# Kernel optimization log

Measured on AMD Instinct MI355X. Metric: run time of the kernel, lower is better.

The kernel has to match this reference:

```python
import jax, jax.numpy as jnp
import numpy as np

D_MODEL, D_STATE, D_CONV, EXPAND = 2048, 16, 4, 2
D_INNER = EXPAND * D_MODEL            # 4096
DT_RANK = -(-D_MODEL // 16)           # 128
B_SZ, L = 2, 1024


def setup_inputs() -> dict:
    key = jax.random.key(0)
    ks = jax.random.split(key, 10)
    s = 0.02
    return {
        "hidden_states": jax.random.normal(ks[0], (B_SZ, L, D_MODEL), jnp.float32),
        "in_proj_w": jax.random.normal(ks[1], (2 * D_INNER, D_MODEL), jnp.float32) * s,
        "conv_w": jax.random.normal(ks[2], (D_INNER, D_CONV), jnp.float32) * 0.1,
        "conv_b": jax.random.normal(ks[3], (D_INNER,), jnp.float32) * 0.1,
        "x_proj_w": jax.random.normal(ks[4], (DT_RANK + 2 * D_STATE, D_INNER), jnp.float32) * s,
        "dt_proj_w": jax.random.normal(ks[5], (D_INNER, DT_RANK), jnp.float32) * s,
        "dt_proj_b": jax.random.normal(ks[6], (D_INNER,), jnp.float32) * 0.1 - 4.0,
        "A": -jax.random.uniform(ks[7], (D_INNER, D_STATE), jnp.float32, 1.0, 16.0),
        "D": jnp.ones((D_INNER,), jnp.float32),
        "out_proj_w": jax.random.normal(ks[8], (D_MODEL, D_INNER), jnp.float32) * s,
    }


def _mamba_forward(hidden_states, in_proj_w, conv_w, conv_b, x_proj_w,
                   dt_proj_w, dt_proj_b, A, D, out_proj_w):
    # in_proj: [B,L,d_model] -> [B,L,2*d_inner]; chunk into x and gate
    proj = jnp.einsum('bld,ed->ble', hidden_states, in_proj_w)
    x, gate = jnp.split(proj, 2, axis=-1)            # each [B,L,d_inner]

    # depthwise causal conv1d over time + SiLU
    xc = x.transpose(0, 2, 1)                        # [B,d_inner,L]
    xc = jax.lax.conv_general_dilated(
        xc, conv_w[:, None, :],                      # kernel [d_inner,1,d_conv]
        window_strides=(1,), padding=[(D_CONV - 1, 0)],
        feature_group_count=D_INNER,
        dimension_numbers=('NCH', 'OIH', 'NCH'))
    xc = jax.nn.silu(xc + conv_b[None, :, None])
    xt = xc.transpose(0, 2, 1)                       # [B,L,d_inner]

    # x_proj -> (dt_rank, d_state, d_state)
    ssm = jnp.einsum('bld,ed->ble', xt, x_proj_w)
    ts, Bm, Cm = jnp.split(ssm, [DT_RANK, DT_RANK + D_STATE], axis=-1)
    dt = jnp.einsum('blr,dr->bld', ts, dt_proj_w)    # dt_proj (skip_bias_add)
    dt = jax.nn.softplus(dt + dt_proj_b)             # delta_softplus with bias

    # selective scan over time
    def step(state, inp):
        dt_t, x_t, B_t, C_t = inp                    # [B,di],[B,di],[B,ds],[B,ds]
        dA = jnp.exp(dt_t[..., None] * A)            # [B,d_inner,d_state]
        dBx = dt_t[..., None] * B_t[:, None, :] * x_t[..., None]
        state = state * dA + dBx
        y = jnp.einsum('bds,bs->bd', state, C_t)
        return state, y

    xs = (dt.transpose(1, 0, 2), xt.transpose(1, 0, 2),
          Bm.transpose(1, 0, 2), Cm.transpose(1, 0, 2))
    state0 = jnp.zeros((hidden_states.shape[0], D_INNER, D_STATE), jnp.float32)
    _, ys = jax.lax.scan(step, state0, xs)           # [L,B,d_inner]
    y = ys.transpose(1, 0, 2) + xt * D               # D skip connection
    y = y * jax.nn.silu(gate)                        # gating (z in selective scan)

    return jnp.einsum('bld,ed->ble', y, out_proj_w)  # out_proj -> [B,L,d_model]


def reference(hidden_states, in_proj_w, conv_w, conv_b, x_proj_w,
              dt_proj_w, dt_proj_b, A, D, out_proj_w):
    return _mamba_forward(hidden_states, in_proj_w, conv_w, conv_b, x_proj_w,
                          dt_proj_w, dt_proj_b, A, D, out_proj_w)
```

## Files before the change

### kernel.cpp

```cpp
#include <hip/hip_runtime.h>
#include <hip/hip_bf16.h>
#include <math.h>

#define B_SZ    2
#define LSEQ    1024
#define D_MODEL 2048
#define D_INNER 4096
#define D_STATE 16
#define DT_RANK 128
#define M_TOK   (B_SZ * LSEQ)
#define NCHUNK  16
#define LCHUNK  (LSEQ / NCHUNK)

typedef __attribute__((ext_vector_type(8))) short bf16x8;
typedef __attribute__((ext_vector_type(4))) float f32x4;

__device__ __forceinline__ float softplusf_(float x) {
    return fmaxf(x, 0.f) + log1pf(expf(-fabsf(x)));
}
__device__ __forceinline__ unsigned f2bf(float f) {
    union { float f; unsigned u; } v; v.f = f;
    const unsigned u = v.u;
    return (u + 0x7fffu + ((u >> 16) & 1u)) >> 16;
}
__device__ __forceinline__ float bf2f(unsigned u) {
    union { unsigned u; float f; } v; v.u = u << 16; return v.f;
}
__device__ __forceinline__ void gload16(const void* g, void* lds) {
    __builtin_amdgcn_global_load_lds(
        (const __attribute__((address_space(1))) void*)g,
        (__attribute__((address_space(3))) void*)lds, 16, 0, 0);
}

__global__ __launch_bounds__(512, 2)
void gemm256_1ph(const ushort* __restrict__ A, int lda,
                 const ushort* __restrict__ B, int ldb,
                 void* __restrict__ Cv, int ldc,
                 void* __restrict__ Cv2,
                 int K, int epi, size_t zstride)
{
    __shared__ ushort Lds[2][2][2][128 * 64];
    const int t    = threadIdx.x;
    const int bm   = blockIdx.y << 8, bn = blockIdx.x << 8;
    const int wave = t >> 6, lane = t & 63;
    const int wm   = wave >> 2;
    const int wn   = wave & 3;
    const int lr   = lane & 15, lh = lane >> 4;
    const int kper  = K / gridDim.z;
    const int kbase = blockIdx.z * kper;
    const int nkt   = kper >> 6;

    const ushort* gsA[2]; const ushort* gsB[2];
    int dof[2];
#pragma unroll
    for (int it = 0; it < 2; ++it) {
        const int flat = t + (it << 9);
        const int row  = flat >> 3, j = flat & 7;
        const int jj   = j ^ (row & 7);
        gsA[it] = A + (size_t)(bm + row) * lda + kbase + jj * 8;
        gsB[it] = B + (size_t)(bn + row) * ldb + kbase + jj * 8;
        dof[it] = flat << 3;
    }

#define STG_A(half, kt, db) do {                                            \
    _Pragma("unroll")                                                       \
    for (int it = 0; it < 2; ++it)                                          \
        gload16(gsA[it] + (size_t)((half) * 128) * lda + (kt) * 64,         \
                &Lds[db][0][half][dof[it]]);                                \
} while (0)
#define STG_B(half, kt, db) do {                                            \
    _Pragma("unroll")                                                       \
    for (int it = 0; it < 2; ++it)                                          \
        gload16(gsB[it] + (size_t)((half) * 128) * ldb + (kt) * 64,         \
                &Lds[db][1][half][dof[it]]);                                \
} while (0)
#define RD_A(db, half) do {                                                 \
    _Pragma("unroll")                                                       \
    for (int mi = 0; mi < 4; ++mi)                                          \
    _Pragma("unroll")                                                       \
    for (int kk = 0; kk < 2; ++kk) {                                        \
        const int row_ = wm * 64 + mi * 16 + lr;                            \
        const int ch_  = ((kk << 2) + lh) ^ (row_ & 7);                     \
        af[mi * 2 + kk] = *(const bf16x8*)((const char*)Lds[db][0][half]    \
                             + row_ * 128 + (ch_ << 4));                    \
    }                                                                       \
} while (0)
#define RD_B(db, half, dst) do {                                            \
    _Pragma("unroll")                                                       \
    for (int nj = 0; nj < 2; ++nj)                                          \
    _Pragma("unroll")                                                       \
    for (int kk = 0; kk < 2; ++kk) {                                        \
        const int row_ = wn * 32 + nj * 16 + lr;                            \
        const int ch_  = ((kk << 2) + lh) ^ (row_ & 7);                     \
        dst[nj * 2 + kk] = *(const bf16x8*)((const char*)Lds[db][1][half]   \
                             + row_ * 128 + (ch_ << 4));                    \
    }                                                                       \
} while (0)
#define MFMA_PAIR(qa, qb, bfa, bfb) do {                                    \
    _Pragma("unroll")                                                       \
    for (int kk = 0; kk < 2; ++kk) {                                        \
        _Pragma("unroll")                                                   \
        for (int mi = 0; mi < 4; ++mi)                                      \
        _Pragma("unroll")                                                   \
        for (int nj = 0; nj < 2; ++nj)                                      \
            acc[qa][mi][nj] = __builtin_amdgcn_mfma_f32_16x16x32_bf16(      \
                af[mi * 2 + kk], bfa[nj * 2 + kk], acc[qa][mi][nj], 0, 0, 0);\
        _Pragma("unroll")                                                   \
        for (int mi = 0; mi < 4; ++mi)                                      \
        _Pragma("unroll")                                                   \
        for (int nj = 0; nj < 2; ++nj)                                      \
            acc[qb][mi][nj] = __builtin_amdgcn_mfma_f32_16x16x32_bf16(      \
                af[mi * 2 + kk], bfb[nj * 2 + kk], acc[qb][mi][nj], 0, 0, 0);\
    }                                                                       \
} while (0)

    f32x4 acc[4][4][2];
#pragma unroll
    for (int q = 0; q < 4; ++q)
#pragma unroll
        for (int i = 0; i < 4; ++i)
#pragma unroll
            for (int j = 0; j < 2; ++j) {
                acc[q][i][j][0] = 0.f; acc[q][i][j][1] = 0.f;
                acc[q][i][j][2] = 0.f; acc[q][i][j][3] = 0.f;
            }

    bf16x8 af[8], bf0[4], bf1[4];

    STG_A(0, 0, 0); STG_B(0, 0, 0); STG_B(1, 0, 0); STG_A(1, 0, 0);
    asm volatile("s_waitcnt vmcnt(0)" ::: "memory");
    __builtin_amdgcn_s_barrier();

    for (int kt = 0; kt < nkt; ++kt) {
        const int db = kt & 1;
        RD_A(db, 0); RD_B(db, 0, bf0); RD_B(db, 1, bf1);
        if (kt + 1 < nkt) {
            STG_A(0, kt + 1, db ^ 1); STG_B(0, kt + 1, db ^ 1);
            STG_B(1, kt + 1, db ^ 1); STG_A(1, kt + 1, db ^ 1);
        }
        MFMA_PAIR(0, 1, bf0, bf1);
        RD_A(db, 1);
        MFMA_PAIR(2, 3, bf1, bf0);
        asm volatile("s_waitcnt vmcnt(0)" ::: "memory");
        __builtin_amdgcn_s_barrier();
    }
#undef STG_A
#undef STG_B
#undef RD_A
#undef RD_B
#undef MFMA_PAIR

    float*  C  = (float*)Cv + (size_t)blockIdx.z * zstride;
    ushort* Cb = (ushort*)Cv;
    ushort* C2 = (ushort*)Cv2;
#pragma unroll
    for (int q = 0; q < 4; ++q) {
        const int mh = q >> 1;
        const int nh = (q == 1 || q == 2) ? 1 : 0;
#pragma unroll
        for (int mi = 0; mi < 4; ++mi) {
#pragma unroll
            for (int nj = 0; nj < 2; ++nj) {
                const int col  = bn + nh * 128 + wn * 32 + nj * 16 + lr;
                const int row0 = bm + mh * 128 + wm * 64 + mi * 16 + (lh << 2);
#pragma unroll
                for (int r = 0; r < 4; ++r) {
                    const float v = acc[q][mi][nj][r];
                    if (epi == 0) {
                        C[(size_t)(row0 + r) * ldc + col] = v;
                    } else {
                        if (col < D_INNER)
                            Cb[(size_t)(row0 + r) * ldc + col] = (ushort)f2bf(v);
                        else
                            C2[(size_t)(row0 + r) * ldc + (col - D_INNER)] = (ushort)f2bf(v);
                    }
                }
            }
        }
    }
}

__global__ __launch_bounds__(512, 4)
void gemm_bf16_bt(const ushort* __restrict__ A, int lda,
                  const ushort* __restrict__ B, int ldb,
                  void* __restrict__ Cv, int ldc,
                  const float* __restrict__ bias,
                  int M, int N, int K, int epi, size_t zstride)
{
    __shared__ ushort As[2][128 * 64];
    __shared__ ushort Bs[2][128 * 64];
    const int t    = threadIdx.x;
    const int bm   = blockIdx.y << 7, bn = blockIdx.x << 7;
    const int wave = t >> 6, lane = t & 63;
    const int wr   = (wave >> 2) << 6;
    const int wc   = (wave & 3) << 5;
    const int lr   = lane & 15, lh = lane >> 4;
    const int kper  = K / gridDim.z;
    const int kbase = blockIdx.z * kper;
    const int nkt   = kper >> 6;

    const ushort* ga[2]; const ushort* gb[2];
    int ldof[2];
#pragma unroll
    for (int it = 0; it < 2; ++it) {
        const int seg = wave + (it << 3);
        const int row = (seg << 3) + (lane >> 3);
        const int jj  = (lane & 7) ^ ((lane >> 3) & 7);
        ga[it] = A + (size_t)(bm + row) * lda + kbase + jj * 8;
        int gn = bn + row; gn = gn < N ? gn : N - 1;
        gb[it] = B + (size_t)gn * ldb + kbase + jj * 8;
        ldof[it] = seg << 9;
    }

#define STAGE(bsel) do {                                                \
    _Pragma("unroll")                                                   \
    for (int it = 0; it < 2; ++it) {                                    \
        gload16(ga[it], &As[bsel][ldof[it]]);                           \
        gload16(gb[it], &Bs[bsel][ldof[it]]);                           \
        ga[it] += 64; gb[it] += 64;                                     \
    }                                                                   \
} while (0)

    f32x4 acc[4][2];
#pragma unroll
    for (int i = 0; i < 4; ++i)
#pragma unroll
        for (int j = 0; j < 2; ++j) {
            acc[i][j][0] = 0.f; acc[i][j][1] = 0.f;
            acc[i][j][2] = 0.f; acc[i][j][3] = 0.f;
        }

    STAGE(0);
    for (int kt = 0; kt < nkt; ++kt) {
        const int cur = kt & 1;
        if (kt + 1 < nkt) {
            STAGE(cur ^ 1);
            asm volatile("s_waitcnt vmcnt(4)" ::: "memory");
        } else {
            asm volatile("s_waitcnt vmcnt(0)" ::: "memory");
        }
        __builtin_amdgcn_s_barrier();

        const char* Ab = (const char*)As[cur];
        const char* Bb = (const char*)Bs[cur];
#pragma unroll
        for (int kk = 0; kk < 2; ++kk) {
            bf16x8 af[4], bf[2];
#pragma unroll
            for (int mi = 0; mi < 4; ++mi) {
                const int row = wr + (mi << 4) + lr;
                const int ch  = ((kk << 2) + lh) ^ (row & 7);
                af[mi] = *(const bf16x8*)(Ab + row * 128 + (ch << 4));
            }
#pragma unroll
            for (int nj = 0; nj < 2; ++nj) {
                const int row = wc + (nj << 4) + lr;
                const int ch  = ((kk << 2) + lh) ^ (row & 7);
                bf[nj] = *(const bf16x8*)(Bb + row * 128 + (ch << 4));
            }
#pragma unroll
            for (int mi = 0; mi < 4; ++mi)
#pragma unroll
                for (int nj = 0; nj < 2; ++nj)
                    acc[mi][nj] = __builtin_amdgcn_mfma_f32_16x16x32_bf16(
                        af[mi], bf[nj], acc[mi][nj], 0, 0, 0);
        }
        __builtin_amdgcn_s_barrier();
    }
#undef STAGE

    float*  C  = (float*)Cv + (size_t)blockIdx.z * zstride;
    ushort* Cb = (ushort*)Cv;
#pragma unroll
    for (int mi = 0; mi < 4; ++mi) {
#pragma unroll
        for (int nj = 0; nj < 2; ++nj) {
            const int col  = bn + wc + (nj << 4) + lr;
            const int row0 = bm + wr + (mi << 4) + (lh << 2);
            if (col < N) {
#pragma unroll
                for (int r = 0; r < 4; ++r) {
                    const float v = acc[mi][nj][r];
                    if (epi == 0)
                        C[(size_t)(row0 + r) * ldc + col] = v;
                    else
                        Cb[(size_t)(row0 + r) * ldc + col] =
                            (ushort)f2bf(softplusf_(v + bias[col]));
                }
            }
        }
    }
}

#define CVT_N_HS   524288
#define CVT_N_INW  2097152
#define CVT1_E0    (CVT_N_HS)
#define CVT1_E1    (CVT1_E0 + CVT_N_INW)

__global__ __launch_bounds__(256)
void cvt_step1(const float* __restrict__ hs,  ushort* __restrict__ hsb,
               const float* __restrict__ inw, ushort* __restrict__ inwb)
{
    for (int i = blockIdx.x * 256 + threadIdx.x; i < CVT1_E1; i += gridDim.x * 256) {
        const float* in; ushort* out; int j;
        if (i < CVT1_E0) { in = hs;  out = hsb;  j = i; }
        else             { in = inw; out = inwb; j = i - CVT1_E0; }
        const float4 v0 = ((const float4*)in)[j * 2];
        const float4 v1 = ((const float4*)in)[j * 2 + 1];
        int4 p;
        p.x = (int)(f2bf(v0.x) | (f2bf(v0.y) << 16));
        p.y = (int)(f2bf(v0.z) | (f2bf(v0.w) << 16));
        p.z = (int)(f2bf(v1.x) | (f2bf(v1.y) << 16));
        p.w = (int)(f2bf(v1.z) | (f2bf(v1.w) << 16));
        ((int4*)out)[j] = p;
    }
}

#define CVT_N_OW   1048576
#define CVT_N_XW   81920
#define CVT_N_DTW  65536
#define CVT4_E0    (CVT_N_OW)
#define CVT4_E1    (CVT4_E0 + CVT_N_XW)
#define CVT4_E2    (CVT4_E1 + CVT_N_DTW)

__global__ __launch_bounds__(256)
void cvt_step4(const float* __restrict__ ow,  ushort* __restrict__ owb,
               const float* __restrict__ xw,  ushort* __restrict__ xwb,
               const float* __restrict__ dtw, ushort* __restrict__ dtwb)
{
    for (int i = blockIdx.x * 256 + threadIdx.x; i < CVT4_E2; i += gridDim.x * 256) {
        const float* in; ushort* out; int j;
        if (i < CVT4_E0)      { in = ow;  out = owb;  j = i; }
        else if (i < CVT4_E1) { in = xw;  out = xwb;  j = i - CVT4_E0; }
        else                  { in = dtw; out = dtwb; j = i - CVT4_E1; }
        const float4 v0 = ((const float4*)in)[j * 2];
        const float4 v1 = ((const float4*)in)[j * 2 + 1];
        int4 p;
        p.x = (int)(f2bf(v0.x) | (f2bf(v0.y) << 16));
        p.y = (int)(f2bf(v0.z) | (f2bf(v0.w) << 16));
        p.z = (int)(f2bf(v1.x) | (f2bf(v1.y) << 16));
        p.w = (int)(f2bf(v1.z) | (f2bf(v1.w) << 16));
        ((int4*)out)[j] = p;
    }
}

__global__ __launch_bounds__(256)
void reduce_out4(const float* __restrict__ part, float* __restrict__ out, int n4)
{
    const int stride = M_TOK * D_MODEL / 4;
    for (int i = blockIdx.x * 256 + threadIdx.x; i < n4; i += gridDim.x * 256) {
        const float4 a = ((const float4*)part)[i];
        const float4 b = ((const float4*)part)[i + stride];
        const float4 c = ((const float4*)part)[i + 2 * stride];
        const float4 d = ((const float4*)part)[i + 3 * stride];
        ((float4*)out)[i] = make_float4(a.x + b.x + c.x + d.x,
                                        a.y + b.y + c.y + d.y,
                                        a.z + b.z + c.z + d.z,
                                        a.w + b.w + c.w + d.w);
    }
}

__global__ __launch_bounds__(256)
void conv_silu_k(const ushort* __restrict__ xraw,
                 const float* __restrict__ cw,
                 const float* __restrict__ cb,
                 ushort* __restrict__ xb)
{
    const int d  = (blockIdx.x << 8) + threadIdx.x;
    const int m0 = blockIdx.y << 6;
    const int l0 = m0 & (LSEQ - 1);
    const float4 w = *(const float4*)&cw[d << 2];
    const float bias = cb[d];
    float x3 = 0.f, x2 = 0.f, x1 = 0.f;
    if (l0 > 0) {
        x3 = bf2f(xraw[(size_t)(m0 - 3) * D_INNER + d]);
        x2 = bf2f(xraw[(size_t)(m0 - 2) * D_INNER + d]);
        x1 = bf2f(xraw[(size_t)(m0 - 1) * D_INNER + d]);
    }
#pragma unroll 4
    for (int i = 0; i < 64; ++i) {
        const size_t m = (size_t)m0 + i;
        const float x0 = bf2f(xraw[m * D_INNER + d]);
        float acc = bias;
        acc = fmaf(w.x, x3, acc);
        acc = fmaf(w.y, x2, acc);
        acc = fmaf(w.z, x1, acc);
        acc = fmaf(w.w, x0, acc);
        const float sg = 1.f / (1.f + expf(-acc));
        xb[m * D_INNER + d] = (ushort)f2bf(acc * sg);
        x3 = x2; x2 = x1; x1 = x0;
    }
}

__global__ __launch_bounds__(256)
void reduce_ssm(const float* __restrict__ part,
                float* __restrict__ ssmf, ushort* __restrict__ ssmb)
{
    const int i = blockIdx.x * 256 + threadIdx.x;
    float v = 0.f;
#pragma unroll
    for (int z = 0; z < 8; ++z) v += part[(size_t)z * (M_TOK * 160) + i];
    ssmf[i] = v;
    ssmb[i] = (ushort)f2bf(v);
}

__global__ __launch_bounds__(256)
void scan_pass1(const ushort* __restrict__ dtp,
                const ushort* __restrict__ xb,
                const float* __restrict__ ssm,
                const float* __restrict__ Ap,
                float* __restrict__ Pc, float* __restrict__ Qc)
{
    const int d = (blockIdx.x << 8) + threadIdx.x;
    const int c = blockIdx.y, b = blockIdx.z;
    float a[16];
    *(float4*)&a[0]  = *(const float4*)&Ap[d * 16];
    *(float4*)&a[4]  = *(const float4*)&Ap[d * 16 + 4];
    *(float4*)&a[8]  = *(const float4*)&Ap[d * 16 + 8];
    *(float4*)&a[12] = *(const float4*)&Ap[d * 16 + 12];
    float q[16];
#pragma unroll
    for (int s = 0; s < 16; ++s) q[s] = 0.f;
    float dtsum = 0.f;
    const size_t m0 = (size_t)b * LSEQ + (size_t)c * LCHUNK;
#pragma unroll 2
    for (int l = 0; l < LCHUNK; ++l) {
        const size_t m = m0 + l;
        const float dt = bf2f(dtp[m * D_INNER + d]);
        const float xv = bf2f(xb[m * D_INNER + d]);
        const float4 B0 = *(const float4*)&ssm[m * 160 + 128];
        const float4 B1 = *(const float4*)&ssm[m * 160 + 132];
        const float4 B2 = *(const float4*)&ssm[m * 160 + 136];
        const float4 B3 = *(const float4*)&ssm[m * 160 + 140];
        const float Bv[16] = {B0.x,B0.y,B0.z,B0.w, B1.x,B1.y,B1.z,B1.w,
                              B2.x,B2.y,B2.z,B2.w, B3.x,B3.y,B3.z,B3.w};
        const float t1 = dt * xv;
#pragma unroll
        for (int s = 0; s < 16; ++s) {
            const float dA = __expf(dt * a[s]);
            q[s] = fmaf(q[s], dA, t1 * Bv[s]);
        }
        dtsum += dt;
    }
    const size_t o = (((size_t)b * D_INNER + d) * NCHUNK + c) * D_STATE;
    float P[16];
#pragma unroll
    for (int s = 0; s < 16; ++s) P[s] = __expf(a[s] * dtsum);
#pragma unroll
    for (int s4 = 0; s4 < 4; ++s4) {
        *(float4*)&Pc[o + s4 * 4] = make_float4(P[s4*4], P[s4*4+1], P[s4*4+2], P[s4*4+3]);
        *(float4*)&Qc[o + s4 * 4] = make_float4(q[s4*4], q[s4*4+1], q[s4*4+2], q[s4*4+3]);
    }
}

__global__ __launch_bounds__(256)
void scan_pass2(const float* __restrict__ Pc, float* __restrict__ Qc)
{
    const int i = blockIdx.x * 256 + threadIdx.x;
    const size_t base = (size_t)(i >> 4) * (NCHUNK * D_STATE) + (i & 15);
    float st = 0.f;
#pragma unroll
    for (int c = 0; c < NCHUNK; ++c) {
        const float P = Pc[base + c * D_STATE];
        const float q = Qc[base + c * D_STATE];
        Qc[base + c * D_STATE] = st;
        st = fmaf(st, P, q);
    }
}

__global__ __launch_bounds__(256)
void scan_pass3(const ushort* __restrict__ dtp,
                ushort* __restrict__ xb,
                const ushort* __restrict__ gb,
                const float* __restrict__ ssm,
                const float* __restrict__ Ap,
                const float* __restrict__ Qc,
                const float* __restrict__ Dp)
{
    const int d = (blockIdx.x << 8) + threadIdx.x;
    const int c = blockIdx.y, b = blockIdx.z;
    float a[16], st[16];
    *(float4*)&a[0]  = *(const float4*)&Ap[d * 16];
    *(float4*)&a[4]  = *(const float4*)&Ap[d * 16 + 4];
    *(float4*)&a[8]  = *(const float4*)&Ap[d * 16 + 8];
    *(float4*)&a[12] = *(const float4*)&Ap[d * 16 + 12];
    const size_t qo = (((size_t)b * D_INNER + d) * NCHUNK + c) * D_STATE;
    *(float4*)&st[0]  = *(const float4*)&Qc[qo];
    *(float4*)&st[4]  = *(const float4*)&Qc[qo + 4];
    *(float4*)&st[8]  = *(const float4*)&Qc[qo + 8];
    *(float4*)&st[12] = *(const float4*)&Qc[qo + 12];
    const float Dd = Dp[d];
    const size_t m0 = (size_t)b * LSEQ + (size_t)c * LCHUNK;
#pragma unroll 2
    for (int l = 0; l < LCHUNK; ++l) {
        const size_t m = m0 + l;
        const float dt = bf2f(dtp[m * D_INNER + d]);
        const float xv = bf2f(xb[m * D_INNER + d]);
        const float gv = bf2f(gb[m * D_INNER + d]);
        const float4 B0 = *(const float4*)&ssm[m * 160 + 128];
        const float4 B1 = *(const float4*)&ssm[m * 160 + 132];
        const float4 B2 = *(const float4*)&ssm[m * 160 + 136];
        const float4 B3 = *(const float4*)&ssm[m * 160 + 140];
        const float4 C0 = *(const float4*)&ssm[m * 160 + 144];
        const float4 C1 = *(const float4*)&ssm[m * 160 + 148];
        const float4 C2 = *(const float4*)&ssm[m * 160 + 152];
        const float4 C3 = *(const float4*)&ssm[m * 160 + 156];
        const float Bv[16] = {B0.x,B0.y,B0.z,B0.w, B1.x,B1.y,B1.z,B1.w,
                              B2.x,B2.y,B2.z,B2.w, B3.x,B3.y,B3.z,B3.w};
        const float Cv[16] = {C0.x,C0.y,C0.z,C0.w, C1.x,C1.y,C1.z,C1.w,
                              C2.x,C2.y,C2.z,C2.w, C3.x,C3.y,C3.z,C3.w};
        const float t1 = dt * xv;
        float y = 0.f;
#pragma unroll
        for (int s = 0; s < 16; ++s) {
            const float dA = __expf(dt * a[s]);
            st[s] = fmaf(st[s], dA, t1 * Bv[s]);
            y = fmaf(st[s], Cv[s], y);
        }
        const float yg  = fmaf(Dd, xv, y);
        const float sig = 1.f / (1.f + expf(-gv));
        xb[m * D_INNER + d] = (ushort)f2bf(yg * (gv * sig));
    }
}

extern "C" void kernel_launch(void* const* d_in, const int* in_sizes, int n_in,
                              void* d_out, int out_size, void* d_ws, size_t ws_size,
                              hipStream_t stream)
{
    (void)in_sizes; (void)n_in; (void)out_size; (void)ws_size;
    const float* hs  = (const float*)d_in[0];
    const float* inw = (const float*)d_in[1];
    const float* cw  = (const float*)d_in[2];
    const float* cb  = (const float*)d_in[3];
    const float* xw  = (const float*)d_in[4];
    const float* dtw = (const float*)d_in[5];
    const float* dtb = (const float*)d_in[6];
    const float* Ap  = (const float*)d_in[7];
    const float* Dp  = (const float*)d_in[8];
    const float* ow  = (const float*)d_in[9];
    float* out = (float*)d_out;

    float*  ws    = (float*)d_ws;
    float*  P     = ws;
    ushort* hsb   = (ushort*)(ws + 0);
    ushort* inwb  = (ushort*)(ws + 2097152);
    ushort* dtb16 = (ushort*)(ws + 0);
    ushort* xwb   = (ushort*)(ws + 4194304);
    ushort* dtwb  = (ushort*)(ws + 4521984);
    float*  ssmf  = ws + 4784128;
    ushort* ssmb  = (ushort*)(ws + 5111808);
    float*  part  = ws + 5275648;
    float*  Pc    = ws + 5275648;
    float*  Qc    = ws + 7372800;
    ushort* pg    = (ushort*)(ws + 10485760);
    ushort* xtb   = (ushort*)(ws + 16777216);
    ushort* xraw  = (ushort*)(ws + 20971520);
    ushort* owb   = (ushort*)(ws + 20971520);

    const dim3 blk(256);
    const dim3 blk512(512);

    cvt_step1<<<dim3(2048), blk, 0, stream>>>(hs, hsb, inw, inwb);

    gemm256_1ph<<<dim3(32, 8, 1), blk512, 0, stream>>>(
        hsb, D_MODEL, inwb, D_MODEL, xraw, D_INNER, pg, D_MODEL, 5, 0);

    conv_silu_k<<<dim3(16, 32), blk, 0, stream>>>(xraw, cw, cb, xtb);

    cvt_step4<<<dim3(2048), blk, 0, stream>>>(ow, owb, xw, xwb, dtw, dtwb);

    gemm_bf16_bt<<<dim3(2, 16, 8), blk512, 0, stream>>>(
        xtb, D_INNER, xwb, D_INNER, part, 160, nullptr,
        M_TOK, 160, D_INNER, 0, (size_t)M_TOK * 160);
    reduce_ssm<<<dim3(1280), blk, 0, stream>>>(part, ssmf, ssmb);

    gemm_bf16_bt<<<dim3(32, 16, 1), blk512, 0, stream>>>(
        ssmb, 160, dtwb, DT_RANK, dtb16, D_INNER, dtb,
        M_TOK, D_INNER, DT_RANK, 1, 0);

    scan_pass1<<<dim3(16, NCHUNK, B_SZ), blk, 0, stream>>>(dtb16, xtb, ssmf, Ap, Pc, Qc);
    scan_pass2<<<dim3((B_SZ * D_INNER * D_STATE) / 256), blk, 0, stream>>>(Pc, Qc);
    scan_pass3<<<dim3(16, NCHUNK, B_SZ), blk, 0, stream>>>(dtb16, xtb, pg, ssmf, Ap, Qc, Dp);

    gemm256_1ph<<<dim3(8, 8, 4), blk512, 0, stream>>>(
        xtb, D_INNER, owb, D_INNER, P, D_MODEL, nullptr,
        D_INNER, 0, (size_t)M_TOK * D_MODEL);
    reduce_out4<<<dim3(1024), blk, 0, stream>>>(P, out, (M_TOK * D_MODEL) / 4);
}
```

Before: 300.7 us.

## Fuse three chunked selective-scan passes into one kernel with LDS carry propagation

Replaces the three-kernel chunked scan (per-chunk local scan, cross-chunk prefix, final scan with output) with a single kernel. Each block owns 16 channels across all 16 chunks and keeps chunk decay and partial states in shared memory. A block-local sequential pass over chunks computes the carry-in states between two barriers. This removes two kernel launches and the global write and re-read of the Pc/Qc chunk-state buffers. In exchange, each wavefront now reads only 16 contiguous channels per token row across four different chunks, so global loads of dt, x and gate are less coalesced.

```diff
diff --git a/kernel.cpp b/kernel.cpp
--- a/kernel.cpp
+++ b/kernel.cpp
@@ -405,24 +405,32 @@
 }
 
 __global__ __launch_bounds__(256)
-void scan_pass1(const ushort* __restrict__ dtp,
-                const ushort* __restrict__ xb,
+void scan_fused(const ushort* __restrict__ dtp,
+                ushort* __restrict__ xb,
+                const ushort* __restrict__ gb,
                 const float* __restrict__ ssm,
                 const float* __restrict__ Ap,
-                float* __restrict__ Pc, float* __restrict__ Qc)
-{
-    const int d = (blockIdx.x << 8) + threadIdx.x;
-    const int c = blockIdx.y, b = blockIdx.z;
+                const float* __restrict__ Dp)
+{
+    __shared__ float Pl[16 * 17 * 16];
+    __shared__ float Ql[16 * 17 * 16];
+    const int t  = threadIdx.x;
+    const int dl = t & 15, c = t >> 4;
+    const int d  = (blockIdx.x << 4) + dl;
+    const int b  = blockIdx.y;
+    const int base = (dl * 17 + c) * 16;
+
     float a[16];
     *(float4*)&a[0]  = *(const float4*)&Ap[d * 16];
     *(float4*)&a[4]  = *(const float4*)&Ap[d * 16 + 4];
     *(float4*)&a[8]  = *(const float4*)&Ap[d * 16 + 8];
     *(float4*)&a[12] = *(const float4*)&Ap[d * 16 + 12];
+    const size_t m0 = (size_t)b * LSEQ + (size_t)c * LCHUNK;
+
     float q[16];
 #pragma unroll
     for (int s = 0; s < 16; ++s) q[s] = 0.f;
     float dtsum = 0.f;
-    const size_t m0 = (size_t)b * LSEQ + (size_t)c * LCHUNK;
 #pragma unroll 2
     for (int l = 0; l < LCHUNK; ++l) {
         const size_t m = m0 + l;
@@ -442,55 +450,38 @@
         }
         dtsum += dt;
     }
-    const size_t o = (((size_t)b * D_INNER + d) * NCHUNK + c) * D_STATE;
-    float P[16];
-#pragma unroll
-    for (int s = 0; s < 16; ++s) P[s] = __expf(a[s] * dtsum);
 #pragma unroll
     for (int s4 = 0; s4 < 4; ++s4) {
-        *(float4*)&Pc[o + s4 * 4] = make_float4(P[s4*4], P[s4*4+1], P[s4*4+2], P[s4*4+3]);
-        *(float4*)&Qc[o + s4 * 4] = make_float4(q[s4*4], q[s4*4+1], q[s4*4+2], q[s4*4+3]);
-    }
-}
-
-__global__ __launch_bounds__(256)
-void scan_pass2(const float* __restrict__ Pc, float* __restrict__ Qc)
-{
-    const int i = blockIdx.x * 256 + threadIdx.x;
-    const size_t base = (size_t)(i >> 4) * (NCHUNK * D_STATE) + (i & 15);
-    float st = 0.f;
-#pragma unroll
-    for (int c = 0; c < NCHUNK; ++c) {
-        const float P = Pc[base + c * D_STATE];
-        const float q = Qc[base + c * D_STATE];
-        Qc[base + c * D_STATE] = st;
-        st = fmaf(st, P, q);
-    }
-}
-
-__global__ __launch_bounds__(256)
-void scan_pass3(const ushort* __restrict__ dtp,
-                ushort* __restrict__ xb,
-                const ushort* __restrict__ gb,
-                const float* __restrict__ ssm,
-                const float* __restrict__ Ap,
-                const float* __restrict__ Qc,
-                const float* __restrict__ Dp)
-{
-    const int d = (blockIdx.x << 8) + threadIdx.x;
-    const int c = blockIdx.y, b = blockIdx.z;
-    float a[16], st[16];
-    *(float4*)&a[0]  = *(const float4*)&Ap[d * 16];
-    *(float4*)&a[4]  = *(const float4*)&Ap[d * 16 + 4];
-    *(float4*)&a[8]  = *(const float4*)&Ap[d * 16 + 8];
-    *(float4*)&a[12] = *(const float4*)&Ap[d * 16 + 12];
-    const size_t qo = (((size_t)b * D_INNER + d) * NCHUNK + c) * D_STATE;
-    *(float4*)&st[0]  = *(const float4*)&Qc[qo];
-    *(float4*)&st[4]  = *(const float4*)&Qc[qo + 4];
-    *(float4*)&st[8]  = *(const float4*)&Qc[qo + 8];
-    *(float4*)&st[12] = *(const float4*)&Qc[qo + 12];
+        float4 Pv;
+        Pv.x = __expf(a[s4 * 4 + 0] * dtsum);
+        Pv.y = __expf(a[s4 * 4 + 1] * dtsum);
+        Pv.z = __expf(a[s4 * 4 + 2] * dtsum);
+        Pv.w = __expf(a[s4 * 4 + 3] * dtsum);
+        *(float4*)&Pl[base + s4 * 4] = Pv;
+        *(float4*)&Ql[base + s4 * 4] = make_float4(q[s4*4], q[s4*4+1],
+                                                   q[s4*4+2], q[s4*4+3]);
+    }
+    __syncthreads();
+
+    {
+        const int dl2 = t >> 4, s2 = t & 15;
+        float st2 = 0.f;
+#pragma unroll
+        for (int c2 = 0; c2 < NCHUNK; ++c2) {
+            const int idx = (dl2 * 17 + c2) * 16 + s2;
+            const float Pv = Pl[idx];
+            const float qv = Ql[idx];
+            Ql[idx] = st2;
+            st2 = fmaf(st2, Pv, qv);
+        }
+    }
+    __syncthreads();
+
+    float st[16];
+#pragma unroll
+    for (int s4 = 0; s4 < 4; ++s4)
+        *(float4*)&st[s4 * 4] = *(const float4*)&Ql[base + s4 * 4];
     const float Dd = Dp[d];
-    const size_t m0 = (size_t)b * LSEQ + (size_t)c * LCHUNK;
 #pragma unroll 2
     for (int l = 0; l < LCHUNK; ++l) {
         const size_t m = m0 + l;
@@ -550,8 +541,6 @@
     float*  ssmf  = ws + 4784128;
     ushort* ssmb  = (ushort*)(ws + 5111808);
     float*  part  = ws + 5275648;
-    float*  Pc    = ws + 5275648;
-    float*  Qc    = ws + 7372800;
     ushort* pg    = (ushort*)(ws + 10485760);
     ushort* xtb   = (ushort*)(ws + 16777216);
     ushort* xraw  = (ushort*)(ws + 20971520);
@@ -578,9 +567,8 @@
         ssmb, 160, dtwb, DT_RANK, dtb16, D_INNER, dtb,
         M_TOK, D_INNER, DT_RANK, 1, 0);
 
-    scan_pass1<<<dim3(16, NCHUNK, B_SZ), blk, 0, stream>>>(dtb16, xtb, ssmf, Ap, Pc, Qc);
-    scan_pass2<<<dim3((B_SZ * D_INNER * D_STATE) / 256), blk, 0, stream>>>(Pc, Qc);
-    scan_pass3<<<dim3(16, NCHUNK, B_SZ), blk, 0, stream>>>(dtb16, xtb, pg, ssmf, Ap, Qc, Dp);
+    scan_fused<<<dim3(D_INNER / 16, B_SZ), blk, 0, stream>>>(
+        dtb16, xtb, pg, ssmf, Ap, Dp);
 
     gemm256_1ph<<<dim3(8, 8, 4), blk512, 0, stream>>>(
         xtb, D_INNER, owb, D_INNER, P, D_MODEL, nullptr,
```

After: 293.3 us. 2.5% less time.
